# Kernel tuning notes

Hardware: AMD Instinct MI355X
Metric: run time of the kernel (lower is better)

The kernel has to match this reference:

```python
import jax, jax.numpy as jnp
import numpy as np

L, B, H, R = 128, 4, 768, 97
LN_EPS = 1e-5


def setup_inputs() -> dict:
    key = jax.random.key(0)
    ks = jax.random.split(key, 8)
    s = 0.02
    return {
        "h_re1": jax.random.normal(ks[0], (L, B, H), jnp.float32),
        "h_re2": jax.random.normal(ks[1], (L, B, H), jnp.float32),
        "mask": jax.random.uniform(ks[2], (L, B), jnp.float32),
        "Wr": jax.random.normal(ks[3], (H, 2 * H), jnp.float32) * s,
        "br": jnp.zeros((H,), jnp.float32),
        "Wh": jax.random.normal(ks[4], (H, 3 * H), jnp.float32) * s,
        "bh": jnp.zeros((H,), jnp.float32),
        "gamma": jnp.ones((H,), jnp.float32),
        "beta": jnp.zeros((H,), jnp.float32),
        "Wo": jax.random.normal(ks[5], (R, H), jnp.float32) * s,
        "bo": jnp.zeros((R,), jnp.float32),
    }


def reference(h_re1, h_re2, mask, Wr, br, Wh, bh, gamma, beta, Wo, bo):
    # h_re1, h_re2: [L, B, H]; mask: [L, B]
    h = h_re2.shape[-1]
    # global context: tanh(Linear(cat(h_re1,h_re2))), max over length -> [B, H]
    g = jnp.tanh(jnp.einsum('lbi,hi->lbh', jnp.concatenate([h_re1, h_re2], axis=-1), Wr) + br)
    g = jnp.max(g, axis=0)  # [B, H]
    # hid2hid(cat(r1, r2, g)) == r1 @ W1.T + r2 @ W2.T + g @ W3.T + b
    # (avoids materializing the [L,L,B,3H] repeat+cat tensor)
    W1, W2, W3 = Wh[:, :h], Wh[:, h:2 * h], Wh[:, 2 * h:]
    a = jnp.einsum('lbi,hi->lbh', h_re2, W1)          # varies over first pair axis
    b2 = jnp.einsum('lbi,hi->lbh', h_re2, W2)         # varies over second pair axis
    gp = jnp.einsum('bi,hi->bh', g, W3) + bh          # constant over pairs
    pre = a[:, None, :, :] + b2[None, :, :, :] + gp   # [L, L, B, H]
    # LayerNorm over last dim (biased variance, as in torch)
    mu = jnp.mean(pre, axis=-1, keepdims=True)
    var = jnp.var(pre, axis=-1, keepdims=True)
    x = (pre - mu) * jax.lax.rsqrt(var + LN_EPS) * gamma + beta
    x = jax.nn.elu(x)  # dropout is identity in eval mode
    out = jax.nn.sigmoid(jnp.einsum('klbh,rh->klbr', x, Wo) + bo)  # [L, L, B, R]
    # pairwise mask: mask_e1 * mask_e2, broadcast over relation dim
    m = mask[:, None, :, None] * mask[None, :, :, None]
    return out * m
```

## Files before the change

### kernel.cpp

```cpp
#include <hip/hip_runtime.h>
#include <hip/hip_bf16.h>
#include <stdint.h>

#define L_ 128
#define B_ 4
#define H_ 768
#define R_ 97
#define LN_EPS 1e-5f

typedef _Float16 f16x8 __attribute__((ext_vector_type(8)));
typedef _Float16 f16x4 __attribute__((ext_vector_type(4)));
typedef _Float16 f16x2 __attribute__((ext_vector_type(2)));
typedef float f32x4 __attribute__((ext_vector_type(4)));

extern "C" __device__ _Float16 __ocml_exp2_f16(_Float16);

__device__ inline f16x8 cvt8(float4 v0, float4 v1) {
  f16x8 o;
  o[0] = (_Float16)v0.x; o[1] = (_Float16)v0.y; o[2] = (_Float16)v0.z; o[3] = (_Float16)v0.w;
  o[4] = (_Float16)v1.x; o[5] = (_Float16)v1.y; o[6] = (_Float16)v1.z; o[7] = (_Float16)v1.w;
  return o;
}

__global__ __launch_bounds__(256) void prep_all(const float* __restrict__ h1,
                                                const float* __restrict__ h2,
                                                const float* __restrict__ Wr,
                                                const float* __restrict__ Wh,
                                                const float* __restrict__ Wo,
                                                const float* __restrict__ gamma,
                                                const float* __restrict__ beta,
                                                _Float16* __restrict__ ccH,
                                                _Float16* __restrict__ BpR,
                                                _Float16* __restrict__ BpW,
                                                _Float16* __restrict__ WoP,
                                                _Float16* __restrict__ gbH,
                                                unsigned int* __restrict__ gmaxU) {
  int blk = blockIdx.x;
  if (blk < 512) {
    const float2* s1 = (const float2*)(h1 + (size_t)blk * H_);
    const float2* s2 = (const float2*)(h2 + (size_t)blk * H_);
    f16x2* d = (f16x2*)(ccH + (size_t)blk * (2 * H_));
    for (int i = threadIdx.x; i < H_ / 2; i += 256) {
      float2 v = s1[i]; f16x2 o; o[0] = (_Float16)v.x; o[1] = (_Float16)v.y; d[i] = o;
    }
    for (int i = threadIdx.x; i < H_ / 2; i += 256) {
      float2 v = s2[i]; f16x2 o; o[0] = (_Float16)v.x; o[1] = (_Float16)v.y; d[H_ / 2 + i] = o;
    }
    return;
  }
  blk -= 512;
  if (blk < 576) {
    int c = blk * 256 + threadIdx.x;
    int l = c & 63, u = c >> 6;
    int nt = u % 48, ks = u / 48;
    int n = nt * 16 + (l & 15);
    int k = ks * 32 + ((l >> 4) << 3);
    const float4* s = (const float4*)(Wr + (size_t)n * 1536 + k);
    *(f16x8*)(BpR + (size_t)c * 8) = cvt8(s[0], s[1]);
    return;
  }
  blk -= 576;
  if (blk < 576) {
    int c = blk * 256 + threadIdx.x;
    int l = c & 63, u = c >> 6;
    int nt = u % 96, ks = u / 96;
    int n = nt * 16 + (l & 15);
    int k = ks * 32 + ((l >> 4) << 3);
    const float* src = (n < 768) ? (Wh + (size_t)n * 2304 + k)
                                 : (Wh + (size_t)(n - 768) * 2304 + 768 + k);
    const float4* s = (const float4*)src;
    *(f16x8*)(BpW + (size_t)c * 8) = cvt8(s[0], s[1]);
    return;
  }
  blk -= 576;
  if (blk < 48) {
    int c = blk * 256 + threadIdx.x;
    int l = c & 63, u = c >> 6;
    int nt = u & 7, ks = u >> 3;
    int n = nt * 16 + (l & 15);
    int k = ks * 32 + ((l >> 4) << 3);
    f16x8 o = {};
    if (n < R_) {
      const float4* s = (const float4*)(Wo + (size_t)n * 768 + k);
      o = cvt8(s[0], s[1]);
    }
    *(f16x8*)(WoP + (size_t)c * 8) = o;
    return;
  }
  blk -= 48;
  if (blk < 3) {
    int i = blk * 256 + threadIdx.x;
    if (i < H_) {
      gbH[i] = (_Float16)gamma[i];
      gbH[H_ + i] = (_Float16)beta[i];
    }
    return;
  }
  blk -= 3;
  int i = blk * 256 + threadIdx.x;
  if (i < B_ * H_) gmaxU[i] = 0u;
}

__global__ __launch_bounds__(256) void gemm_g(const _Float16* __restrict__ A,
                                              const _Float16* __restrict__ BpR,
                                              const float* __restrict__ br,
                                              unsigned int* __restrict__ gmaxU) {
  int w = threadIdx.x >> 6, l = threadIdx.x & 63;
  int nb = blockIdx.x, mb = blockIdx.y;
  int row0 = mb * 32 + (w & 1) * 16;
  int nt0 = nb * 4 + (w >> 1) * 2;
  const f16x8* ap = (const f16x8*)(A + (size_t)(row0 + (l & 15)) * 1536 + (l >> 4) * 8);
  const f16x8* bp = (const f16x8*)(BpR + ((size_t)nt0 * 64 + l) * 8);
  f32x4 acc0 = {}, acc1 = {};
  f16x8 ac = ap[0], b0c = bp[0], b1c = bp[64];
  for (int ks = 0; ks < 48; ++ks) {
    f16x8 an = {}, b0n = {}, b1n = {};
    if (ks < 47) {
      an = ap[(ks + 1) * 4];
      b0n = bp[(size_t)(ks + 1) * 3072];
      b1n = bp[(size_t)(ks + 1) * 3072 + 64];
    }
    acc0 = __builtin_amdgcn_mfma_f32_16x16x32_f16(ac, b0c, acc0, 0, 0, 0);
    acc1 = __builtin_amdgcn_mfma_f32_16x16x32_f16(ac, b1c, acc1, 0, 0, 0);
    ac = an; b0c = b0n; b1c = b1n;
  }
#pragma unroll
  for (int q = 0; q < 2; ++q) {
    f32x4 acc = q ? acc1 : acc0;
    int col = nb * 64 + (w >> 1) * 32 + q * 16 + (l & 15);
#pragma unroll
    for (int r = 0; r < 4; ++r) {
      int row = row0 + (l >> 4) * 4 + r;
      float t = tanhf(acc[r] + br[col]) + 1.0f;
      atomicMax(&gmaxU[(row & 3) * H_ + col], __float_as_uint(t));
    }
  }
}

__global__ __launch_bounds__(256) void gemm_ab(const _Float16* __restrict__ ccH,
                                               const _Float16* __restrict__ BpW,
                                               _Float16* __restrict__ aH,
                                               _Float16* __restrict__ bH) {
  int w = threadIdx.x >> 6, l = threadIdx.x & 63;
  int nb = blockIdx.x, mb = blockIdx.y;
  int row0 = mb * 32 + (w & 1) * 16;
  int nt0 = nb * 4 + (w >> 1) * 2;
  const f16x8* ap = (const f16x8*)(ccH + (size_t)(row0 + (l & 15)) * 1536 + 768 + (l >> 4) * 8);
  const f16x8* bp = (const f16x8*)(BpW + ((size_t)nt0 * 64 + l) * 8);
  f32x4 acc0 = {}, acc1 = {};
  f16x8 ac = ap[0], b0c = bp[0], b1c = bp[64];
  for (int ks = 0; ks < 24; ++ks) {
    f16x8 an = {}, b0n = {}, b1n = {};
    if (ks < 23) {
      an = ap[(ks + 1) * 4];
      b0n = bp[(size_t)(ks + 1) * 6144];
      b1n = bp[(size_t)(ks + 1) * 6144 + 64];
    }
    acc0 = __builtin_amdgcn_mfma_f32_16x16x32_f16(ac, b0c, acc0, 0, 0, 0);
    acc1 = __builtin_amdgcn_mfma_f32_16x16x32_f16(ac, b1c, acc1, 0, 0, 0);
    ac = an; b0c = b0n; b1c = b1n;
  }
#pragma unroll
  for (int q = 0; q < 2; ++q) {
    f32x4 acc = q ? acc1 : acc0;
    int col = nb * 64 + (w >> 1) * 32 + q * 16 + (l & 15);
#pragma unroll
    for (int r = 0; r < 4; ++r) {
      int row = row0 + (l >> 4) * 4 + r;
      float v = acc[r];
      if (col < 768) aH[(size_t)row * H_ + col] = (_Float16)v;
      else           bH[(size_t)row * H_ + (col - 768)] = (_Float16)v;
    }
  }
}

__global__ __launch_bounds__(256) void gp_kernel(const float* __restrict__ Wh,
                                                 const unsigned int* __restrict__ gmaxU,
                                                 const float* __restrict__ bh,
                                                 float* __restrict__ gpv) {
  int n = blockIdx.x;
  int w = threadIdx.x >> 6, l = threadIdx.x & 63;
  const float* wr = Wh + (size_t)n * 2304 + 1536;
  const unsigned int* gm = gmaxU + (size_t)w * H_;
  float s = 0.f;
#pragma unroll
  for (int t = 0; t < 12; ++t) {
    int i = l + 64 * t;
    s += wr[i] * (__uint_as_float(gm[i]) - 1.0f);
  }
#pragma unroll
  for (int off = 32; off; off >>= 1) s += __shfl_xor(s, off);
  if (l == 0) gpv[(size_t)w * H_ + n] = s + bh[n];
}

__global__ __launch_bounds__(256) void stats(const _Float16* __restrict__ aH,
                                             const _Float16* __restrict__ bH,
                                             const float* __restrict__ gpv,
                                             _Float16* __restrict__ aH2,
                                             float* __restrict__ S,
                                             float* __restrict__ Q) {
  int r = blockIdx.x * 4 + (threadIdx.x >> 6);
  int l = threadIdx.x & 63;
  float s = 0.f, q = 0.f;
  if (r < 512) {
    int b = r & 3;
    const f16x4* ap = (const f16x4*)(aH + (size_t)r * H_);
    const float4* gp4 = (const float4*)(gpv + (size_t)b * H_);
    f16x4* op = (f16x4*)(aH2 + (size_t)r * H_);
#pragma unroll
    for (int t = 0; t < 3; ++t) {
      int i = t * 64 + l;
      f16x4 av = ap[i];
      float4 g4 = gp4[i];
      f16x4 o;
      o[0] = (_Float16)((float)av[0] + g4.x);
      o[1] = (_Float16)((float)av[1] + g4.y);
      o[2] = (_Float16)((float)av[2] + g4.z);
      o[3] = (_Float16)((float)av[3] + g4.w);
      op[i] = o;
#pragma unroll
      for (int j = 0; j < 4; ++j) { float y = (float)o[j]; s += y; q += y * y; }
    }
  } else {
    const f16x4* bp = (const f16x4*)(bH + (size_t)(r - 512) * H_);
#pragma unroll
    for (int t = 0; t < 3; ++t) {
      f16x4 bv = bp[t * 64 + l];
#pragma unroll
      for (int j = 0; j < 4; ++j) { float y = (float)bv[j]; s += y; q += y * y; }
    }
  }
#pragma unroll
  for (int off = 32; off; off >>= 1) {
    s += __shfl_xor(s, off);
    q += __shfl_xor(q, off);
  }
  if (l == 0) { S[r] = s; Q[r] = q; }
}

__global__ __launch_bounds__(256) void dotab(const _Float16* __restrict__ aH2,
                                             const _Float16* __restrict__ bH,
                                             const float* __restrict__ S,
                                             const float* __restrict__ Q,
                                             float* __restrict__ mu_arr,
                                             float* __restrict__ rs_arr) {
  int w = threadIdx.x >> 6, l = threadIdx.x & 63;
  int ltq = blockIdx.x, kt = blockIdx.y, b = blockIdx.z;
  int lt = ltq * 4 + w;
  const f16x8* ap = (const f16x8*)(aH2 + ((size_t)(kt * 16 + (l & 15)) * 4 + b) * H_ + (l >> 4) * 8);
  const f16x8* bp = (const f16x8*)(bH + ((size_t)(lt * 16 + (l & 15)) * 4 + b) * H_ + (l >> 4) * 8);
  f32x4 acc = {};
  f16x8 a0 = ap[0], b0 = bp[0], a1 = ap[4], b1 = bp[4];
  for (int ks = 0; ks < 24; ++ks) {
    f16x8 a2 = {}, b2 = {};
    if (ks < 22) { a2 = ap[(ks + 2) * 4]; b2 = bp[(ks + 2) * 4]; }
    acc = __builtin_amdgcn_mfma_f32_16x16x32_f16(a0, b0, acc, 0, 0, 0);
    a0 = a1; b0 = b1; a1 = a2; b1 = b2;
  }
#pragma unroll
  for (int r = 0; r < 4; ++r) {
    int k = kt * 16 + (l >> 4) * 4 + r;
    int lg = lt * 16 + (l & 15);
    int arow = k * 4 + b, brow = lg * 4 + b;
    float mu = (S[arow] + S[512 + brow]) * (1.f / H_);
    float q2 = Q[arow] + Q[512 + brow] + 2.f * acc[r];
    float var = fmaxf(q2 * (1.f / H_) - mu * mu, 0.f);
    float rs = rsqrtf(var + LN_EPS);
    size_t idx = (size_t)k * 512 + (size_t)lg * 4 + b;
    mu_arr[idx] = mu;
    rs_arr[idx] = rs;
  }
}

__global__ __launch_bounds__(256) void fused2(const _Float16* __restrict__ aH2,
                                              const _Float16* __restrict__ bH,
                                              const _Float16* __restrict__ gbH,
                                              const _Float16* __restrict__ WoP,
                                              const float* __restrict__ bo,
                                              const float* __restrict__ mask,
                                              const float* __restrict__ mu_arr,
                                              const float* __restrict__ rs_arr,
                                              float* __restrict__ out) {
  __shared__ __align__(16) _Float16 WoLds[2][4096];
  int tid = threadIdx.x, w = tid >> 6, l = tid & 63;
  int m0 = blockIdx.x * 64;
  int myrow = m0 + w * 16 + (l & 15);
  int b = myrow & 3, li = (myrow >> 2) & 127, kk = myrow >> 9;
  const f16x8* ap = (const f16x8*)(aH2 + ((size_t)kk * 4 + b) * H_ + (l >> 4) * 8);
  const f16x8* bp = (const f16x8*)(bH + ((size_t)li * 4 + b) * H_ + (l >> 4) * 8);
  const f16x8* gp8 = (const f16x8*)(gbH + (l >> 4) * 8);
  const f16x8* be8 = (const f16x8*)(gbH + H_ + (l >> 4) * 8);
  float mu = mu_arr[myrow], rs = rs_arr[myrow];
  _Float16 muh = (_Float16)mu, rsh = (_Float16)rs;
  _Float16 l2e = (_Float16)1.44269504f;
  f16x8 mu8, rs8, zero8, one8, l2e8;
#pragma unroll
  for (int j = 0; j < 8; ++j) {
    mu8[j] = muh; rs8[j] = rsh;
    zero8[j] = (_Float16)0.f; one8[j] = (_Float16)1.f; l2e8[j] = l2e;
  }

  const uint4* wog = (const uint4*)WoP;
  uint4* lds0 = (uint4*)&WoLds[0][0];
  lds0[tid] = wog[tid];
  lds0[256 + tid] = wog[256 + tid];
  __syncthreads();

  f16x8 a8 = ap[0], b8 = bp[0], g8 = gp8[0], e8 = be8[0];

  f32x4 acc[7] = {};
  for (int ks = 0; ks < 24; ++ks) {
    int cur = ks & 1;
    uint4 wo0 = {}, wo1 = {};
    f16x8 an = {}, bn = {}, gn = {}, en = {};
    if (ks < 23) {
      wo0 = wog[(ks + 1) * 512 + tid];
      wo1 = wog[(ks + 1) * 512 + 256 + tid];
      an = ap[(ks + 1) * 4];
      bn = bp[(ks + 1) * 4];
      gn = gp8[(ks + 1) * 4];
      en = be8[(ks + 1) * 4];
    }
    f16x8 x = a8 + b8;
    f16x8 c1 = rs8 * g8;
    f16x8 yv = (x - mu8) * c1 + e8;
    f16x8 y2 = yv * l2e8;
    f16x8 ex;
#pragma unroll
    for (int j = 0; j < 8; ++j) ex[j] = __ocml_exp2_f16(y2[j]);
    ex = ex - one8;
    f16x8 av = __builtin_elementwise_max(yv, zero8) + __builtin_elementwise_min(ex, zero8);
    __syncthreads();
    if (ks < 23) {
      uint4* d = (uint4*)&WoLds[cur ^ 1][0];
      d[tid] = wo0;
      d[256 + tid] = wo1;
    }
    __syncthreads();
    const f16x8* bvp = (const f16x8*)&WoLds[cur][0];
#pragma unroll
    for (int q = 0; q < 7; ++q) {
      f16x8 bv = bvp[q * 64 + l];
      acc[q] = __builtin_amdgcn_mfma_f32_16x16x32_f16(av, bv, acc[q], 0, 0, 0);
    }
    a8 = an; b8 = bn; g8 = gn; e8 = en;
  }
  float mv[4];
#pragma unroll
  for (int r = 0; r < 4; ++r) {
    int row = m0 + w * 16 + (l >> 4) * 4 + r;
    int bb = row & 3, ll = (row >> 2) & 127, kx = row >> 9;
    mv[r] = mask[kx * 4 + bb] * mask[ll * 4 + bb];
  }
#pragma unroll
  for (int q = 0; q < 7; ++q) {
    int col = q * 16 + (l & 15);
    if (col < R_) {
      float bov = bo[col];
#pragma unroll
      for (int r = 0; r < 4; ++r) {
        int row = m0 + w * 16 + (l >> 4) * 4 + r;
        float z = acc[q][r] + bov;
        out[(size_t)row * R_ + col] = mv[r] / (1.f + __expf(-z));
      }
    }
  }
}

extern "C" void kernel_launch(void* const* d_in, const int* in_sizes, int n_in,
                              void* d_out, int out_size, void* d_ws, size_t ws_size,
                              hipStream_t stream) {
  const float* h1    = (const float*)d_in[0];
  const float* h2    = (const float*)d_in[1];
  const float* mask  = (const float*)d_in[2];
  const float* Wr    = (const float*)d_in[3];
  const float* br    = (const float*)d_in[4];
  const float* Wh    = (const float*)d_in[5];
  const float* bh    = (const float*)d_in[6];
  const float* gamma = (const float*)d_in[7];
  const float* beta  = (const float*)d_in[8];
  const float* Wo    = (const float*)d_in[9];
  const float* bo    = (const float*)d_in[10];
  float* out = (float*)d_out;
  char* ws = (char*)d_ws;

  _Float16* ccH = (_Float16*)ws;                    size_t off = 512 * 1536 * 2;
  _Float16* BpR = (_Float16*)(ws + off);            off += (size_t)1536 * 768 * 2;
  _Float16* BpW = (_Float16*)(ws + off);            off += (size_t)768 * 1536 * 2;
  _Float16* WoP = (_Float16*)(ws + off);            off += 768 * 128 * 2;
  _Float16* gbH = (_Float16*)(ws + off);            off += 4096;
  _Float16* aH  = (_Float16*)(ws + off);            off += 512 * 768 * 2;
  _Float16* bH  = (_Float16*)(ws + off);            off += 512 * 768 * 2;
  _Float16* aH2 = (_Float16*)(ws + off);            off += 512 * 768 * 2;
  unsigned int* gmaxU = (unsigned int*)(ws + off);  off += 3072 * 4;
  float* gpv = (float*)(ws + off);                  off += 3072 * 4;
  float* S   = (float*)(ws + off);                  off += 1024 * 4;
  float* Q   = (float*)(ws + off);                  off += 1024 * 4;
  float* mu_arr = (float*)(ws + off);               off += 65536 * 4;
  float* rs_arr = (float*)(ws + off);               off += 65536 * 4;

  prep_all<<<512 + 576 + 576 + 48 + 3 + 12, 256, 0, stream>>>(h1, h2, Wr, Wh, Wo, gamma, beta,
                                                              ccH, BpR, BpW, WoP, gbH, gmaxU);

  gemm_g<<<dim3(12, 16), 256, 0, stream>>>(ccH, BpR, br, gmaxU);
  gemm_ab<<<dim3(24, 16), 256, 0, stream>>>(ccH, BpW, aH, bH);
  gp_kernel<<<768, 256, 0, stream>>>(Wh, gmaxU, bh, gpv);
  stats<<<256, 256, 0, stream>>>(aH, bH, gpv, aH2, S, Q);
  dotab<<<dim3(2, 8, 4), 256, 0, stream>>>(aH2, bH, S, Q, mu_arr, rs_arr);

  fused2<<<1024, 256, 0, stream>>>(aH2, bH, gbH, WoP, bo, mask, mu_arr, rs_arr, out);
}
```

Measured before the change: 102.8 us.

## Merge the two projection GEMMs into one launch and triple-buffer Wo in LDS

The independent gemm_g and gemm_ab kernels are merged into one launch of 576 blocks that dispatches on block index, removing a launch boundary and letting both GEMMs share the GPU at the same time. In fused2, the Wo staging buffer grows from two to three LDS slots, with prefetch two steps ahead, so one of the two __syncthreads per k-step can be dropped. This cuts per-iteration barrier cost and launch overhead, at the price of 8 KB more LDS per block, which may lower occupancy.

```diff
diff --git a/kernel.cpp b/kernel.cpp
--- a/kernel.cpp
+++ b/kernel.cpp
@@ -101,12 +101,12 @@
   if (i < B_ * H_) gmaxU[i] = 0u;
 }
 
-__global__ __launch_bounds__(256) void gemm_g(const _Float16* __restrict__ A,
-                                              const _Float16* __restrict__ BpR,
-                                              const float* __restrict__ br,
-                                              unsigned int* __restrict__ gmaxU) {
+__device__ __forceinline__ void gemm_g_tile(int nb, int mb,
+                                            const _Float16* __restrict__ A,
+                                            const _Float16* __restrict__ BpR,
+                                            const float* __restrict__ br,
+                                            unsigned int* __restrict__ gmaxU) {
   int w = threadIdx.x >> 6, l = threadIdx.x & 63;
-  int nb = blockIdx.x, mb = blockIdx.y;
   int row0 = mb * 32 + (w & 1) * 16;
   int nt0 = nb * 4 + (w >> 1) * 2;
   const f16x8* ap = (const f16x8*)(A + (size_t)(row0 + (l & 15)) * 1536 + (l >> 4) * 8);
@@ -137,12 +137,12 @@
   }
 }
 
-__global__ __launch_bounds__(256) void gemm_ab(const _Float16* __restrict__ ccH,
-                                               const _Float16* __restrict__ BpW,
-                                               _Float16* __restrict__ aH,
-                                               _Float16* __restrict__ bH) {
+__device__ __forceinline__ void gemm_ab_tile(int nb, int mb,
+                                             const _Float16* __restrict__ ccH,
+                                             const _Float16* __restrict__ BpW,
+                                             _Float16* __restrict__ aH,
+                                             _Float16* __restrict__ bH) {
   int w = threadIdx.x >> 6, l = threadIdx.x & 63;
-  int nb = blockIdx.x, mb = blockIdx.y;
   int row0 = mb * 32 + (w & 1) * 16;
   int nt0 = nb * 4 + (w >> 1) * 2;
   const f16x8* ap = (const f16x8*)(ccH + (size_t)(row0 + (l & 15)) * 1536 + 768 + (l >> 4) * 8);
@@ -171,6 +171,22 @@
       if (col < 768) aH[(size_t)row * H_ + col] = (_Float16)v;
       else           bH[(size_t)row * H_ + (col - 768)] = (_Float16)v;
     }
+  }
+}
+
+__global__ __launch_bounds__(256) void gemm_both(const _Float16* __restrict__ ccH,
+                                                 const _Float16* __restrict__ BpR,
+                                                 const _Float16* __restrict__ BpW,
+                                                 const float* __restrict__ br,
+                                                 unsigned int* __restrict__ gmaxU,
+                                                 _Float16* __restrict__ aH,
+                                                 _Float16* __restrict__ bH) {
+  int bid = blockIdx.x;
+  if (bid < 192) {
+    gemm_g_tile(bid % 12, bid / 12, ccH, BpR, br, gmaxU);
+  } else {
+    int j2 = bid - 192;
+    gemm_ab_tile(j2 % 24, j2 / 24, ccH, BpW, aH, bH);
   }
 }
 
@@ -281,7 +297,7 @@
                                               const float* __restrict__ mu_arr,
                                               const float* __restrict__ rs_arr,
                                               float* __restrict__ out) {
-  __shared__ __align__(16) _Float16 WoLds[2][4096];
+  __shared__ __align__(16) _Float16 WoLds[3][4096];
   int tid = threadIdx.x, w = tid >> 6, l = tid & 63;
   int m0 = blockIdx.x * 64;
   int myrow = m0 + w * 16 + (l & 15);
@@ -301,21 +317,26 @@
   }
 
   const uint4* wog = (const uint4*)WoP;
-  uint4* lds0 = (uint4*)&WoLds[0][0];
-  lds0[tid] = wog[tid];
-  lds0[256 + tid] = wog[256 + tid];
+  {
+    uint4* d0 = (uint4*)&WoLds[0][0];
+    uint4* d1 = (uint4*)&WoLds[1][0];
+    d0[tid] = wog[tid];            d0[256 + tid] = wog[256 + tid];
+    d1[tid] = wog[512 + tid];      d1[256 + tid] = wog[512 + 256 + tid];
+  }
   __syncthreads();
 
   f16x8 a8 = ap[0], b8 = bp[0], g8 = gp8[0], e8 = be8[0];
 
+  int cur = 0, wt = 2;
   f32x4 acc[7] = {};
   for (int ks = 0; ks < 24; ++ks) {
-    int cur = ks & 1;
     uint4 wo0 = {}, wo1 = {};
     f16x8 an = {}, bn = {}, gn = {}, en = {};
+    if (ks < 22) {
+      wo0 = wog[(ks + 2) * 512 + tid];
+      wo1 = wog[(ks + 2) * 512 + 256 + tid];
+    }
     if (ks < 23) {
-      wo0 = wog[(ks + 1) * 512 + tid];
-      wo1 = wog[(ks + 1) * 512 + 256 + tid];
       an = ap[(ks + 1) * 4];
       bn = bp[(ks + 1) * 4];
       gn = gp8[(ks + 1) * 4];
@@ -331,12 +352,11 @@
     ex = ex - one8;
     f16x8 av = __builtin_elementwise_max(yv, zero8) + __builtin_elementwise_min(ex, zero8);
     __syncthreads();
-    if (ks < 23) {
-      uint4* d = (uint4*)&WoLds[cur ^ 1][0];
+    if (ks < 22) {
+      uint4* d = (uint4*)&WoLds[wt][0];
       d[tid] = wo0;
       d[256 + tid] = wo1;
     }
-    __syncthreads();
     const f16x8* bvp = (const f16x8*)&WoLds[cur][0];
 #pragma unroll
     for (int q = 0; q < 7; ++q) {
@@ -344,6 +364,8 @@
       acc[q] = __builtin_amdgcn_mfma_f32_16x16x32_f16(av, bv, acc[q], 0, 0, 0);
     }
     a8 = an; b8 = bn; g8 = gn; e8 = en;
+    cur = (cur == 2) ? 0 : cur + 1;
+    wt = (wt == 2) ? 0 : wt + 1;
   }
   float mv[4];
 #pragma unroll
@@ -402,8 +424,7 @@
   prep_all<<<512 + 576 + 576 + 48 + 3 + 12, 256, 0, stream>>>(h1, h2, Wr, Wh, Wo, gamma, beta,
                                                               ccH, BpR, BpW, WoP, gbH, gmaxU);
 
-  gemm_g<<<dim3(12, 16), 256, 0, stream>>>(ccH, BpR, br, gmaxU);
-  gemm_ab<<<dim3(24, 16), 256, 0, stream>>>(ccH, BpW, aH, bH);
+  gemm_both<<<576, 256, 0, stream>>>(ccH, BpR, BpW, br, gmaxU, aH, bH);
   gp_kernel<<<768, 256, 0, stream>>>(Wh, gmaxU, bh, gpv);
   stats<<<256, 256, 0, stream>>>(aH, bH, gpv, aH2, S, Q);
   dotab<<<dim3(2, 8, 4), 256, 0, stream>>>(aH2, bH, S, Q, mu_arr, rs_arr);
```

After: 92.51 us. 10.0% less time.
